# Optimization experiments

Measured on AMD Instinct MI355X. Metric: run time of the kernel, lower is better.

Reference implementation:

```python
import jax, jax.numpy as jnp
import numpy as np
from jax.scipy.special import logsumexp

GAMMA = 1.0  # smoothing parameter
B, T1, T2, D_FEAT = 32, 512, 512, 128


def setup_inputs() -> dict:
    key = jax.random.key(0)
    k1, k2 = jax.random.split(key)
    x = jax.random.normal(k1, (B, T1, D_FEAT), dtype=jnp.float32)
    y = jax.random.normal(k2, (B, T2, D_FEAT), dtype=jnp.float32)
    return {"x": x, "y": y}


def _cosine_dist(x, y):
    # F.normalize(p=2, dim=-1) with eps=1e-12 clamp on the norm
    xn = x / jnp.maximum(jnp.linalg.norm(x, axis=-1, keepdims=True), 1e-12)
    yn = y / jnp.maximum(jnp.linalg.norm(y, axis=-1, keepdims=True), 1e-12)
    return 1.0 - jnp.einsum("btd,bsd->bts", xn, yn)  # [B, T1, T2]


def _soft_dtw(D):
    # Anti-diagonal wavefront DP with soft-min (logsumexp) recurrence.
    b, t1, t2 = D.shape
    R0 = jnp.full((b, t1 + 1, t2 + 1), jnp.inf, dtype=D.dtype).at[:, 0, 0].set(0.0)
    i = jnp.arange(1, t1 + 1)  # fixed-length row indices for every diagonal

    def step(R, k):
        j = k - i                      # column index on anti-diagonal k
        valid = (j >= 1) & (j <= t2)
        jc = jnp.clip(j, 0, t2)        # safe R column index (== j when valid)
        jd = jnp.clip(j - 1, 0, t2)    # safe R column index for j-1
        jm = jnp.clip(j - 1, 0, t2 - 1)
        cost = D[:, i - 1, jm]                 # [B, T1]
        r_diag = R[:, i - 1, jd]
        r_left = R[:, i, jd]
        r_up = R[:, i - 1, jc]
        stacked = jnp.stack([r_diag, r_left, r_up])  # [3, B, T1]
        # mask invalid lanes to 0 so logsumexp never sees all -inf (NaN-safe)
        safe = jnp.where(valid[None, None, :], stacked, 0.0)
        soft_min = -GAMMA * logsumexp(-safe / GAMMA, axis=0)
        old = R[:, i, jc]
        val = jnp.where(valid[None, :], cost + soft_min, old)
        R = R.at[:, i, jc].set(val)
        return R, None

    R, _ = jax.lax.scan(step, R0, jnp.arange(2, t1 + t2 + 1))
    return R[:, t1, t2]  # [B]


def reference(x, y):
    D = _cosine_dist(x, y)
    return _soft_dtw(D)
```

## Files before the change

### kernel.cpp

```cpp
#include <hip/hip_runtime.h>
#include <hip/hip_bf16.h>
#include <cstdint>


#define BT      32
#define TLEN    512
#define DF      128
#define NDIAG   1023
#define BIGV    1e30f
#define INV_LN2 1.44269504088896340f
#define LN2     0.69314718055994531f

#define KC    32
#define SPADX 68
#define SPADY 132

__global__ __launch_bounds__(256) void sdtw_gemm_skew(const float* __restrict__ x,
                                                      const float* __restrict__ y,
                                                      float* __restrict__ skew) {
    __shared__ float smem[8320];
    __shared__ float rsx[64], rsy[128];
    float* xs = smem;
    float* ys = smem + KC * SPADX;

    const int b  = blockIdx.z;
    const int r0 = blockIdx.y * 64;
    const int c0 = blockIdx.x * 128;
    const int tid = threadIdx.x;
    const int tx = tid & 15, ty = tid >> 4;

    const float* xb = x + ((size_t)b * TLEN + r0) * DF;
    const float* yb = y + ((size_t)b * TLEN + c0) * DF;

    float acc[4][8];
    #pragma unroll
    for (int i = 0; i < 4; ++i)
        #pragma unroll
        for (int j = 0; j < 8; ++j) acc[i][j] = 0.0f;

    float psx[2] = {0, 0}, psy[4] = {0, 0, 0, 0};

    float4 rx[2], ry[4];
    #pragma unroll
    for (int i = 0; i < 2; ++i) {
        int g = tid + i * 256, row = g >> 3, kq = g & 7;
        rx[i] = *reinterpret_cast<const float4*>(xb + (size_t)row * DF + kq * 4);
    }
    #pragma unroll
    for (int i = 0; i < 4; ++i) {
        int g = tid + i * 256, row = g >> 3, kq = g & 7;
        ry[i] = *reinterpret_cast<const float4*>(yb + (size_t)row * DF + kq * 4);
    }

    for (int kb = 0; kb < DF; kb += KC) {
        __syncthreads();
        #pragma unroll
        for (int i = 0; i < 2; ++i) {
            int g = tid + i * 256, row = g >> 3, kq = g & 7;
            xs[(kq * 4 + 0) * SPADX + row] = rx[i].x;
            xs[(kq * 4 + 1) * SPADX + row] = rx[i].y;
            xs[(kq * 4 + 2) * SPADX + row] = rx[i].z;
            xs[(kq * 4 + 3) * SPADX + row] = rx[i].w;
            psx[i] = fmaf(rx[i].x, rx[i].x, psx[i]);
            psx[i] = fmaf(rx[i].y, rx[i].y, psx[i]);
            psx[i] = fmaf(rx[i].z, rx[i].z, psx[i]);
            psx[i] = fmaf(rx[i].w, rx[i].w, psx[i]);
        }
        #pragma unroll
        for (int i = 0; i < 4; ++i) {
            int g = tid + i * 256, row = g >> 3, kq = g & 7;
            ys[(kq * 4 + 0) * SPADY + row] = ry[i].x;
            ys[(kq * 4 + 1) * SPADY + row] = ry[i].y;
            ys[(kq * 4 + 2) * SPADY + row] = ry[i].z;
            ys[(kq * 4 + 3) * SPADY + row] = ry[i].w;
            psy[i] = fmaf(ry[i].x, ry[i].x, psy[i]);
            psy[i] = fmaf(ry[i].y, ry[i].y, psy[i]);
            psy[i] = fmaf(ry[i].z, ry[i].z, psy[i]);
            psy[i] = fmaf(ry[i].w, ry[i].w, psy[i]);
        }
        __syncthreads();
        if (kb + KC < DF) {
            #pragma unroll
            for (int i = 0; i < 2; ++i) {
                int g = tid + i * 256, row = g >> 3, kq = g & 7;
                rx[i] = *reinterpret_cast<const float4*>(xb + (size_t)row * DF + (kb + KC) + kq * 4);
            }
            #pragma unroll
            for (int i = 0; i < 4; ++i) {
                int g = tid + i * 256, row = g >> 3, kq = g & 7;
                ry[i] = *reinterpret_cast<const float4*>(yb + (size_t)row * DF + (kb + KC) + kq * 4);
            }
        }
        #pragma unroll
        for (int k = 0; k < KC; ++k) {
            float ax[4], ay[8];
            *reinterpret_cast<float4*>(&ax[0]) = *reinterpret_cast<const float4*>(&xs[k * SPADX + ty * 4]);
            *reinterpret_cast<float4*>(&ay[0]) = *reinterpret_cast<const float4*>(&ys[k * SPADY + tx * 8]);
            *reinterpret_cast<float4*>(&ay[4]) = *reinterpret_cast<const float4*>(&ys[k * SPADY + tx * 8 + 4]);
            #pragma unroll
            for (int i = 0; i < 4; ++i)
                #pragma unroll
                for (int j = 0; j < 8; ++j)
                    acc[i][j] = fmaf(ax[i], ay[j], acc[i][j]);
        }
    }

    #pragma unroll
    for (int o = 1; o <= 4; o <<= 1) {
        psx[0] += __shfl_xor(psx[0], o);
        psx[1] += __shfl_xor(psx[1], o);
        psy[0] += __shfl_xor(psy[0], o);
        psy[1] += __shfl_xor(psy[1], o);
        psy[2] += __shfl_xor(psy[2], o);
        psy[3] += __shfl_xor(psy[3], o);
    }
    if ((tid & 7) == 0) {
        #pragma unroll
        for (int i = 0; i < 2; ++i) rsx[(tid + i * 256) >> 3] = psx[i];
        #pragma unroll
        for (int i = 0; i < 4; ++i) rsy[(tid + i * 256) >> 3] = psy[i];
    }

    __syncthreads();
    float rn[4], cn[8];
    #pragma unroll
    for (int i = 0; i < 4; ++i) rn[i] = 1.0f / fmaxf(sqrtf(rsx[ty * 4 + i]), 1e-12f);
    #pragma unroll
    for (int j = 0; j < 8; ++j) cn[j] = 1.0f / fmaxf(sqrtf(rsy[tx * 8 + j]), 1e-12f);

    float* cs = smem;
    #pragma unroll
    for (int i = 0; i < 4; ++i)
        #pragma unroll
        for (int j = 0; j < 8; ++j)
            cs[(ty * 4 + i) * 130 + tx * 8 + j] =
                (1.0f - acc[i][j] * rn[i] * cn[j]) * INV_LN2;
    __syncthreads();

    float* sk = skew + (size_t)b * (NDIAG * TLEN);
    const int wv = tid >> 6, l = tid & 63;
    for (int dd = wv; dd < 191; dd += 4) {
        int lo = max(0, dd - 127), hi = min(63, dd);
        int rl = lo + l;
        if (rl <= hi)
            sk[(size_t)(r0 + c0 + dd) * TLEN + r0 + rl] = cs[rl * 129 + dd];
    }
}


__device__ __forceinline__ int clampi(int v) {
    return v < 0 ? 0 : (v > NDIAG - 1 ? NDIAG - 1 : v);
}

__device__ __forceinline__ float dpp_shr1_old(float old, float x) {
    return __builtin_bit_cast(float,
        __builtin_amdgcn_update_dpp(__builtin_bit_cast(int, old),
                                    __builtin_bit_cast(int, x),
                                    0x138 , 0xF, 0xF, false));
}

#define PH(s, CC, PN, PO, NQC, MASKED, CLAMPED)                                \
  {                                                                            \
    float up_ = dpp_shr1_old(bd_up, PN);                   \
    float dg_ = dgs;                            \
    float m_   = fminf(fminf(dg_, PN), up_);                                   \
    float mid_ = __builtin_amdgcn_fmed3f(dg_, PN, up_);                        \
    float mx_  = fmaxf(fmaxf(dg_, PN), up_);                                   \
    float e_   = 1.0f + __builtin_amdgcn_exp2f(m_ - mid_)                      \
                      + __builtin_amdgcn_exp2f(m_ - mx_);                      \
    float v_   = CC + m_ - __builtin_amdgcn_logf(e_);                          \
    PO = (MASKED) ? (((unsigned)(vb0 + (s)) < 512u) ? v_ : vBig) : v_;         \
    if (((s) & 3) == 0) bq.x = PO;                                             \
    if (((s) & 3) == 1) bq.y = PO;                                             \
    if (((s) & 3) == 2) bq.z = PO;                                             \
    if (((s) & 3) == 3) { bq.w = PO;                                           \
      if (lt == 63) bnd4[c + 1][(q0 + ((s) >> 2)) & 7] = bq; }                 \
    bd_up = (NQC);                                                             \
    dgs = up_;                                                                 \
    { int kl_ = kd0 + (s) + 8; if (CLAMPED) kl_ = clampi(kl_);                 \
      CC = skb[(size_t)kl_ * TLEN]; }                                          \
  }

#define SEG_BODY(MASKED, CLAMPED)                                              \
    PH(0,  c0, P, Q, nq0.x, MASKED, CLAMPED) PH(1,  c1, Q, P, nq0.y, MASKED, CLAMPED) \
    PH(2,  c2, P, Q, nq0.z, MASKED, CLAMPED) PH(3,  c3, Q, P, nq0.w, MASKED, CLAMPED) \
    PH(4,  c4, P, Q, nq1.x, MASKED, CLAMPED) PH(5,  c5, Q, P, nq1.y, MASKED, CLAMPED) \
    PH(6,  c6, P, Q, nq1.z, MASKED, CLAMPED) PH(7,  c7, Q, P, nq1.w, MASKED, CLAMPED) \
    PH(8,  c0, P, Q, nq2.x, MASKED, CLAMPED) PH(9,  c1, Q, P, nq2.y, MASKED, CLAMPED) \
    PH(10, c2, P, Q, nq2.z, MASKED, CLAMPED) PH(11, c3, Q, P, nq2.w, MASKED, CLAMPED) \
    PH(12, c4, P, Q, nq3.x, MASKED, CLAMPED) PH(13, c5, Q, P, nq3.y, MASKED, CLAMPED) \
    PH(14, c6, P, Q, nq3.z, MASKED, CLAMPED) PH(15, c7, Q, P, nq3.w, MASKED, CLAMPED)

#define PRIME(K)                                                               \
    c0 = skb[(size_t)clampi((K) + 0) * TLEN];                                  \
    c1 = skb[(size_t)clampi((K) + 1) * TLEN];                                  \
    c2 = skb[(size_t)clampi((K) + 2) * TLEN];                                  \
    c3 = skb[(size_t)clampi((K) + 3) * TLEN];                                  \
    c4 = skb[(size_t)clampi((K) + 4) * TLEN];                                  \
    c5 = skb[(size_t)clampi((K) + 5) * TLEN];                                  \
    c6 = skb[(size_t)clampi((K) + 6) * TLEN];                                  \
    c7 = skb[(size_t)clampi((K) + 7) * TLEN];

__global__ __launch_bounds__(512) void sdtw_dp(const float* __restrict__ skew,
                                               float* __restrict__ out) {
    const int b   = blockIdx.x;
    const int tid = threadIdx.x;
    const int ww  = tid >> 6;
    const int c   = ((ww & 3) << 1) | (ww >> 2);
    const int lt  = tid & 63;
    const int row = 64 * c + lt;
    const float* skb = skew + (size_t)b * (NDIAG * TLEN) + row;

    __shared__ float4 bnd4[9][8];
    if (tid < 288) ((float*)bnd4)[tid] = BIGV;

    float P = BIGV, Q = BIGV;
    float vBig  = BIGV;
    float bd_up = BIGV;
    float dgs   = (tid == 0) ? 0.0f : BIGV;
    float4 bq = make_float4(BIGV, BIGV, BIGV, BIGV);

    __syncthreads();

    float c0, c1, c2, c3, c4, c5, c6, c7;
    PRIME(-16 * c)

    for (int s = 0; s < 71; ++s) {
        const int sw  = s - 5 * c;
        const int kd0 = 16 * (s - c);
        const int q0  = (kd0 >> 2) & 7;
        const int vb0 = kd0 - row;

        if (sw >= -1 && sw <= 35) {
            float4 nq0 = bnd4[c][q0];
            float4 nq1 = bnd4[c][(q0 + 1) & 7];
            float4 nq2 = bnd4[c][(q0 + 2) & 7];
            float4 nq3 = bnd4[c][(q0 + 3) & 7];
            if (sw == -1) { PRIME(kd0) }
            if (sw >= 4 && sw <= 31) { SEG_BODY(0, 0) }
            else                     { SEG_BODY(1, 1) }
        } else {
            if (lt == 63) {
                float4 bigq = make_float4(BIGV, BIGV, BIGV, BIGV);
                bnd4[c + 1][q0]           = bigq;
                bnd4[c + 1][(q0 + 1) & 7] = bigq;
                bnd4[c + 1][(q0 + 2) & 7] = bigq;
                bnd4[c + 1][(q0 + 3) & 7] = bigq;
            }
        }
        __syncthreads();
    }

    if (tid == 511) out[b] = Q * LN2;
}

extern "C" void kernel_launch(void* const* d_in, const int* in_sizes, int n_in,
                              void* d_out, int out_size, void* d_ws, size_t ws_size,
                              hipStream_t stream) {
    const float* x = (const float*)d_in[0];
    const float* y = (const float*)d_in[1];
    float* outp = (float*)d_out;

    float* skew = (float*)d_ws;

    sdtw_gemm_skew<<<dim3(4, 8, BT), dim3(256), 0, stream>>>(x, y, skew);
    sdtw_dp<<<dim3(BT), dim3(512), 0, stream>>>(skew, outp);
}
```

Baseline: 139.3 us.

## Store cost matrix row-major instead of anti-diagonal skewed layout

The GEMM kernel now writes the scaled cosine-distance matrix straight to a row-major [B,T1,T2] buffer with float4 stores. This drops the shared-memory staging and the scattered skewed write. The DP kernel reads each lane's cost from its own row at column vb0+s, clamped, instead of from the skewed diagonal buffer. The workspace shrinks and the GEMM epilogue gets simpler, but DP loads are now strided across lanes (each lane on a different row) rather than coalesced along a diagonal, which can hurt the latency-bound DP loop.

```diff
diff --git a/kernel.cpp b/kernel.cpp
--- a/kernel.cpp
+++ b/kernel.cpp
@@ -6,7 +6,6 @@
 #define BT      32
 #define TLEN    512
 #define DF      128
-#define NDIAG   1023
 #define BIGV    1e30f
 #define INV_LN2 1.44269504088896340f
 #define LN2     0.69314718055994531f
@@ -15,10 +14,10 @@
 #define SPADX 68
 #define SPADY 132
 
-__global__ __launch_bounds__(256) void sdtw_gemm_skew(const float* __restrict__ x,
-                                                      const float* __restrict__ y,
-                                                      float* __restrict__ skew) {
-    __shared__ float smem[8320];
+__global__ __launch_bounds__(256) void sdtw_gemm(const float* __restrict__ x,
+                                                 const float* __restrict__ y,
+                                                 float* __restrict__ D) {
+    __shared__ float smem[6400];
     __shared__ float rsx[64], rsy[128];
     float* xs = smem;
     float* ys = smem + KC * SPADX;
@@ -128,29 +127,23 @@
     #pragma unroll
     for (int j = 0; j < 8; ++j) cn[j] = 1.0f / fmaxf(sqrtf(rsy[tx * 8 + j]), 1e-12f);
 
-    float* cs = smem;
-    #pragma unroll
-    for (int i = 0; i < 4; ++i)
-        #pragma unroll
-        for (int j = 0; j < 8; ++j)
-            cs[(ty * 4 + i) * 130 + tx * 8 + j] =
-                (1.0f - acc[i][j] * rn[i] * cn[j]) * INV_LN2;
-    __syncthreads();
-
-    float* sk = skew + (size_t)b * (NDIAG * TLEN);
-    const int wv = tid >> 6, l = tid & 63;
-    for (int dd = wv; dd < 191; dd += 4) {
-        int lo = max(0, dd - 127), hi = min(63, dd);
-        int rl = lo + l;
-        if (rl <= hi)
-            sk[(size_t)(r0 + c0 + dd) * TLEN + r0 + rl] = cs[rl * 129 + dd];
-    }
-}
-
-
-__device__ __forceinline__ int clampi(int v) {
-    return v < 0 ? 0 : (v > NDIAG - 1 ? NDIAG - 1 : v);
-}
+    float* Db = D + ((size_t)b * TLEN + r0) * TLEN + c0;
+    #pragma unroll
+    for (int i = 0; i < 4; ++i) {
+        float4 v0, v1;
+        v0.x = (1.0f - acc[i][0] * rn[i] * cn[0]) * INV_LN2;
+        v0.y = (1.0f - acc[i][1] * rn[i] * cn[1]) * INV_LN2;
+        v0.z = (1.0f - acc[i][2] * rn[i] * cn[2]) * INV_LN2;
+        v0.w = (1.0f - acc[i][3] * rn[i] * cn[3]) * INV_LN2;
+        v1.x = (1.0f - acc[i][4] * rn[i] * cn[4]) * INV_LN2;
+        v1.y = (1.0f - acc[i][5] * rn[i] * cn[5]) * INV_LN2;
+        v1.z = (1.0f - acc[i][6] * rn[i] * cn[6]) * INV_LN2;
+        v1.w = (1.0f - acc[i][7] * rn[i] * cn[7]) * INV_LN2;
+        *reinterpret_cast<float4*>(Db + (size_t)(ty * 4 + i) * TLEN + tx * 8)     = v0;
+        *reinterpret_cast<float4*>(Db + (size_t)(ty * 4 + i) * TLEN + tx * 8 + 4) = v1;
+    }
+}
+
 
 __device__ __forceinline__ float dpp_shr1_old(float old, float x) {
     return __builtin_bit_cast(float,
@@ -159,7 +152,11 @@
                                     0x138 , 0xF, 0xF, false));
 }
 
-#define PH(s, CC, PN, PO, NQC, MASKED, CLAMPED)                                \
+__device__ __forceinline__ int clampj(int v) {
+    return v < 0 ? 0 : (v > TLEN - 1 ? TLEN - 1 : v);
+}
+
+#define PH(s, CC, PN, PO, NQC, MASKED)                                         \
   {                                                                            \
     float up_ = dpp_shr1_old(bd_up, PN);                   \
     float dg_ = dgs;                            \
@@ -177,31 +174,30 @@
       if (lt == 63) bnd4[c + 1][(q0 + ((s) >> 2)) & 7] = bq; }                 \
     bd_up = (NQC);                                                             \
     dgs = up_;                                                                 \
-    { int kl_ = kd0 + (s) + 8; if (CLAMPED) kl_ = clampi(kl_);                 \
-      CC = skb[(size_t)kl_ * TLEN]; }                                          \
+    CC = skb[clampj(vb0 + (s) + 8)];                                           \
   }
 
-#define SEG_BODY(MASKED, CLAMPED)                                              \
-    PH(0,  c0, P, Q, nq0.x, MASKED, CLAMPED) PH(1,  c1, Q, P, nq0.y, MASKED, CLAMPED) \
-    PH(2,  c2, P, Q, nq0.z, MASKED, CLAMPED) PH(3,  c3, Q, P, nq0.w, MASKED, CLAMPED) \
-    PH(4,  c4, P, Q, nq1.x, MASKED, CLAMPED) PH(5,  c5, Q, P, nq1.y, MASKED, CLAMPED) \
-    PH(6,  c6, P, Q, nq1.z, MASKED, CLAMPED) PH(7,  c7, Q, P, nq1.w, MASKED, CLAMPED) \
-    PH(8,  c0, P, Q, nq2.x, MASKED, CLAMPED) PH(9,  c1, Q, P, nq2.y, MASKED, CLAMPED) \
-    PH(10, c2, P, Q, nq2.z, MASKED, CLAMPED) PH(11, c3, Q, P, nq2.w, MASKED, CLAMPED) \
-    PH(12, c4, P, Q, nq3.x, MASKED, CLAMPED) PH(13, c5, Q, P, nq3.y, MASKED, CLAMPED) \
-    PH(14, c6, P, Q, nq3.z, MASKED, CLAMPED) PH(15, c7, Q, P, nq3.w, MASKED, CLAMPED)
-
-#define PRIME(K)                                                               \
-    c0 = skb[(size_t)clampi((K) + 0) * TLEN];                                  \
-    c1 = skb[(size_t)clampi((K) + 1) * TLEN];                                  \
-    c2 = skb[(size_t)clampi((K) + 2) * TLEN];                                  \
-    c3 = skb[(size_t)clampi((K) + 3) * TLEN];                                  \
-    c4 = skb[(size_t)clampi((K) + 4) * TLEN];                                  \
-    c5 = skb[(size_t)clampi((K) + 5) * TLEN];                                  \
-    c6 = skb[(size_t)clampi((K) + 6) * TLEN];                                  \
-    c7 = skb[(size_t)clampi((K) + 7) * TLEN];
-
-__global__ __launch_bounds__(512) void sdtw_dp(const float* __restrict__ skew,
+#define SEG_BODY(MASKED)                                                       \
+    PH(0,  c0, P, Q, nq0.x, MASKED) PH(1,  c1, Q, P, nq0.y, MASKED)            \
+    PH(2,  c2, P, Q, nq0.z, MASKED) PH(3,  c3, Q, P, nq0.w, MASKED)            \
+    PH(4,  c4, P, Q, nq1.x, MASKED) PH(5,  c5, Q, P, nq1.y, MASKED)            \
+    PH(6,  c6, P, Q, nq1.z, MASKED) PH(7,  c7, Q, P, nq1.w, MASKED)            \
+    PH(8,  c0, P, Q, nq2.x, MASKED) PH(9,  c1, Q, P, nq2.y, MASKED)            \
+    PH(10, c2, P, Q, nq2.z, MASKED) PH(11, c3, Q, P, nq2.w, MASKED)            \
+    PH(12, c4, P, Q, nq3.x, MASKED) PH(13, c5, Q, P, nq3.y, MASKED)            \
+    PH(14, c6, P, Q, nq3.z, MASKED) PH(15, c7, Q, P, nq3.w, MASKED)
+
+#define PRIME_J(VB)                                                            \
+    c0 = skb[clampj((VB) + 0)];                                                \
+    c1 = skb[clampj((VB) + 1)];                                                \
+    c2 = skb[clampj((VB) + 2)];                                                \
+    c3 = skb[clampj((VB) + 3)];                                                \
+    c4 = skb[clampj((VB) + 4)];                                                \
+    c5 = skb[clampj((VB) + 5)];                                                \
+    c6 = skb[clampj((VB) + 6)];                                                \
+    c7 = skb[clampj((VB) + 7)];
+
+__global__ __launch_bounds__(512) void sdtw_dp(const float* __restrict__ D,
                                                float* __restrict__ out) {
     const int b   = blockIdx.x;
     const int tid = threadIdx.x;
@@ -209,7 +205,7 @@
     const int c   = ((ww & 3) << 1) | (ww >> 2);
     const int lt  = tid & 63;
     const int row = 64 * c + lt;
-    const float* skb = skew + (size_t)b * (NDIAG * TLEN) + row;
+    const float* skb = D + ((size_t)b * TLEN + row) * TLEN;
 
     __shared__ float4 bnd4[9][8];
     if (tid < 288) ((float*)bnd4)[tid] = BIGV;
@@ -223,7 +219,7 @@
     __syncthreads();
 
     float c0, c1, c2, c3, c4, c5, c6, c7;
-    PRIME(-16 * c)
+    PRIME_J(-row)
 
     for (int s = 0; s < 71; ++s) {
         const int sw  = s - 5 * c;
@@ -236,9 +232,9 @@
             float4 nq1 = bnd4[c][(q0 + 1) & 7];
             float4 nq2 = bnd4[c][(q0 + 2) & 7];
             float4 nq3 = bnd4[c][(q0 + 3) & 7];
-            if (sw == -1) { PRIME(kd0) }
-            if (sw >= 4 && sw <= 31) { SEG_BODY(0, 0) }
-            else                     { SEG_BODY(1, 1) }
+            if (sw == -1) { PRIME_J(vb0) }
+            if (sw >= 4 && sw <= 31) { SEG_BODY(0) }
+            else                     { SEG_BODY(1) }
         } else {
             if (lt == 63) {
                 float4 bigq = make_float4(BIGV, BIGV, BIGV, BIGV);
@@ -261,8 +257,8 @@
     const float* y = (const float*)d_in[1];
     float* outp = (float*)d_out;
 
-    float* skew = (float*)d_ws;
-
-    sdtw_gemm_skew<<<dim3(4, 8, BT), dim3(256), 0, stream>>>(x, y, skew);
-    sdtw_dp<<<dim3(BT), dim3(512), 0, stream>>>(skew, outp);
-}
+    float* D = (float*)d_ws;
+
+    sdtw_gemm<<<dim3(4, 8, BT), dim3(256), 0, stream>>>(x, y, D);
+    sdtw_dp<<<dim3(BT), dim3(512), 0, stream>>>(D, outp);
+}
```

Result: slower. 182.9 us (+31.3%).
